# Performance work log

Hardware: AMD Instinct MI355X
Metric: run time of the kernel (lower is better)

The kernel has to match this reference:

```python
import jax, jax.numpy as jnp
import numpy as np
from jax import lax

OBS, ACT, H, VOX = 2264, 32, 4096, 216  # voxel tail is 6*6*6


def _conv3d(v, w, b):
    # v: [1,1,6,6,6], w: [1,1,3,3,3] (OIDHW), SAME padding, stride 1
    y = lax.conv_general_dilated(v, w, window_strides=(1, 1, 1), padding='SAME',
                                 dimension_numbers=('NCDHW', 'OIDHW', 'NCDHW'))
    return jax.nn.relu(y + b.reshape(1, -1, 1, 1, 1))


def setup_inputs() -> dict:
    key = jax.random.key(0)
    ks = jax.random.split(key, 24)
    s = 0.05
    inp = {'x': jax.random.normal(ks[0], (1, OBS), dtype=jnp.float32)}
    # six Conv3d(1,1,3) kernels + biases
    for i in range(6):
        inp[f'cw{i}'] = jax.random.normal(ks[1 + i], (1, 1, 3, 3, 3), dtype=jnp.float32) * s
        inp[f'cb{i}'] = jax.random.normal(ks[7 + i], (1,), dtype=jnp.float32) * s
    # MLP: Linear(OBS->H), Linear(H->H), Linear(H->ACT); torch layout W:[out,in]
    inp['W0'] = jax.random.normal(ks[13], (H, OBS), dtype=jnp.float32) * 0.02
    inp['b0'] = jnp.zeros((H,), jnp.float32)
    inp['W1'] = jax.random.normal(ks[14], (H, H), dtype=jnp.float32) * 0.02
    inp['b1'] = jnp.zeros((H,), jnp.float32)
    inp['W2'] = jax.random.normal(ks[15], (ACT, H), dtype=jnp.float32) * 0.02
    inp['b2'] = jnp.zeros((ACT,), jnp.float32)
    # default transformations (in_shift=0, in_scale=1, out_shift=0, out_scale=1)
    inp['in_shift'] = jnp.zeros((OBS,), jnp.float32)
    inp['in_scale'] = jnp.ones((OBS,), jnp.float32)
    inp['out_shift'] = jnp.zeros((ACT,), jnp.float32)
    inp['out_scale'] = jnp.ones((ACT,), jnp.float32)
    return inp


def reference(x, cw0, cw1, cw2, cw3, cw4, cw5, cb0, cb1, cb2, cb3, cb4, cb5,
              W0, b0, W1, b1, W2, b2, in_shift, in_scale, out_shift, out_scale):
    v = x[:, -VOX:].reshape(1, 1, 6, 6, 6)
    for w, b in ((cw0, cb0), (cw1, cb1), (cw2, cb2), (cw3, cb3), (cw4, cb4), (cw5, cb5)):
        v = _conv3d(v, w, b)
    out = jnp.concatenate([x[:, :-VOX], v.reshape(1, VOX)], axis=1)
    out = (out - in_shift) / (in_scale + 1e-8)
    out = jnp.tanh(out @ W0.T + b0)
    out = jnp.tanh(out @ W1.T + b1)
    out = out @ W2.T + b2
    return out * out_scale + out_shift
```

## Files before the change

### kernel.cpp

```cpp
#include <hip/hip_runtime.h>
#include <math.h>

#define OBS 2264
#define ACT 32
#define HID 4096
#define VOX 216
#define PRE (OBS - VOX)

__global__ __launch_bounds__(256) void conv_norm_kernel(
    const float* __restrict__ x,
    const float* __restrict__ cw0, const float* __restrict__ cb0,
    const float* __restrict__ cw1, const float* __restrict__ cb1,
    const float* __restrict__ cw2, const float* __restrict__ cb2,
    const float* __restrict__ cw3, const float* __restrict__ cb3,
    const float* __restrict__ cw4, const float* __restrict__ cb4,
    const float* __restrict__ cw5, const float* __restrict__ cb5,
    const float* __restrict__ in_shift, const float* __restrict__ in_scale,
    float* __restrict__ u)
{
    __shared__ float vb[2][VOX];
    const int tid = threadIdx.x;

    if (tid < VOX) vb[0][tid] = x[PRE + tid];
    __syncthreads();

    const float* ws[6] = {cw0, cw1, cw2, cw3, cw4, cw5};
    const float* bs[6] = {cb0, cb1, cb2, cb3, cb4, cb5};

    int cur = 0;
    for (int l = 0; l < 6; ++l) {
        float acc = 0.f;
        if (tid < VOX) {
            const int d = tid / 36;
            const int h = (tid / 6) % 6;
            const int w = tid % 6;
            const float* k = ws[l];
            acc = bs[l][0];
            #pragma unroll
            for (int kd = 0; kd < 3; ++kd) {
                const int dd = d + kd - 1;
                if (dd < 0 || dd > 5) continue;
                #pragma unroll
                for (int kh = 0; kh < 3; ++kh) {
                    const int hh = h + kh - 1;
                    if (hh < 0 || hh > 5) continue;
                    #pragma unroll
                    for (int kw = 0; kw < 3; ++kw) {
                        const int ww = w + kw - 1;
                        if (ww < 0 || ww > 5) continue;
                        acc += k[kd * 9 + kh * 3 + kw] * vb[cur][dd * 36 + hh * 6 + ww];
                    }
                }
            }
            acc = fmaxf(acc, 0.f);
            vb[cur ^ 1][tid] = acc;
        }
        cur ^= 1;
        __syncthreads();
    }

    for (int i = tid; i < OBS; i += 256) {
        const float val = (i < PRE) ? x[i] : vb[cur][i - PRE];
        u[i] = (val - in_shift[i]) / (in_scale[i] + 1e-8f);
    }
}

template<int NIN, bool DO_TANH>
__global__ __launch_bounds__(256) void gemv_kernel(
    const float* __restrict__ W, const float* __restrict__ b,
    const float* __restrict__ u, float* __restrict__ out)
{
    constexpr int N4 = NIN / 4;
    const int row = blockIdx.x;
    const int tid = threadIdx.x;
    const float4* __restrict__ Wr = reinterpret_cast<const float4*>(W + (size_t)row * NIN);
    const float4* __restrict__ u4 = reinterpret_cast<const float4*>(u);

    float acc = 0.f;
    for (int j = tid; j < N4; j += 256) {
        const float4 wv = Wr[j];
        const float4 uv = u4[j];
        acc += wv.x * uv.x + wv.y * uv.y + wv.z * uv.z + wv.w * uv.w;
    }
    #pragma unroll
    for (int off = 32; off > 0; off >>= 1) acc += __shfl_down(acc, off, 64);

    __shared__ float part[4];
    if ((tid & 63) == 0) part[tid >> 6] = acc;
    __syncthreads();
    if (tid == 0) {
        float s = part[0] + part[1] + part[2] + part[3] + b[row];
        out[row] = DO_TANH ? tanhf(s) : s;
    }
}

__global__ __launch_bounds__(256) void gemv_out_kernel(
    const float* __restrict__ W, const float* __restrict__ b,
    const float* __restrict__ u,
    const float* __restrict__ oscale, const float* __restrict__ oshift,
    float* __restrict__ out)
{
    constexpr int N4 = HID / 4;
    const int row = blockIdx.x;
    const int tid = threadIdx.x;
    const float4* __restrict__ Wr = reinterpret_cast<const float4*>(W + (size_t)row * HID);
    const float4* __restrict__ u4 = reinterpret_cast<const float4*>(u);

    float acc = 0.f;
    for (int j = tid; j < N4; j += 256) {
        const float4 wv = Wr[j];
        const float4 uv = u4[j];
        acc += wv.x * uv.x + wv.y * uv.y + wv.z * uv.z + wv.w * uv.w;
    }
    #pragma unroll
    for (int off = 32; off > 0; off >>= 1) acc += __shfl_down(acc, off, 64);

    __shared__ float part[4];
    if ((tid & 63) == 0) part[tid >> 6] = acc;
    __syncthreads();
    if (tid == 0) {
        float s = part[0] + part[1] + part[2] + part[3] + b[row];
        out[row] = s * oscale[row] + oshift[row];
    }
}

extern "C" void kernel_launch(void* const* d_in, const int* in_sizes, int n_in,
                              void* d_out, int out_size, void* d_ws, size_t ws_size,
                              hipStream_t stream) {
    const float* x = (const float*)d_in[0];

    const float* cw[6];
    const float* cb[6];
    if (in_sizes[2] == 1) {
        for (int i = 0; i < 6; ++i) {
            cw[i] = (const float*)d_in[1 + 2 * i];
            cb[i] = (const float*)d_in[2 + 2 * i];
        }
    } else {
        for (int i = 0; i < 6; ++i) {
            cw[i] = (const float*)d_in[1 + i];
            cb[i] = (const float*)d_in[7 + i];
        }
    }
    const float* W0       = (const float*)d_in[13];
    const float* b0       = (const float*)d_in[14];
    const float* W1       = (const float*)d_in[15];
    const float* b1       = (const float*)d_in[16];
    const float* W2       = (const float*)d_in[17];
    const float* b2       = (const float*)d_in[18];
    const float* in_shift = (const float*)d_in[19];
    const float* in_scale = (const float*)d_in[20];
    const float* oshift   = (const float*)d_in[21];
    const float* oscale   = (const float*)d_in[22];

    float* ws = (float*)d_ws;
    float* u  = ws;
    float* h0 = ws + 2304;
    float* h1 = ws + 6400;
    float* y  = (float*)d_out;

    conv_norm_kernel<<<1, 256, 0, stream>>>(
        x, cw[0], cb[0], cw[1], cb[1], cw[2], cb[2],
        cw[3], cb[3], cw[4], cb[4], cw[5], cb[5],
        in_shift, in_scale, u);

    gemv_kernel<OBS, true><<<HID, 256, 0, stream>>>(W0, b0, u, h0);
    gemv_kernel<HID, true><<<HID, 256, 0, stream>>>(W1, b1, h0, h1);
    gemv_out_kernel<<<ACT, 256, 0, stream>>>(W2, b2, h1, oscale, oshift, y);
}
```

Measured before the change: 42.32 us.

## Fuse conv/normalization prologue into first GEMV with per-block recompute

The conv3d stack and input normalization are folded into the first GEMV kernel: each of the 4096 blocks recomputes the conv layers and normalized input into shared memory, then does its row dot product. This removes one kernel launch and the global round trip for the normalized vector. The cost is redundant conv and normalization work plus several barriers in every block. The remaining HID-length GEMV loops also get an unroll hint.

```diff
diff --git a/kernel.cpp b/kernel.cpp
--- a/kernel.cpp
+++ b/kernel.cpp
@@ -6,8 +6,10 @@
 #define HID 4096
 #define VOX 216
 #define PRE (OBS - VOX)
+#define N4_OBS (OBS / 4)
+#define N4_HID (HID / 4)
 
-__global__ __launch_bounds__(256) void conv_norm_kernel(
+__global__ __launch_bounds__(256) void fused0_kernel(
     const float* __restrict__ x,
     const float* __restrict__ cw0, const float* __restrict__ cb0,
     const float* __restrict__ cw1, const float* __restrict__ cb1,
@@ -16,9 +18,13 @@
     const float* __restrict__ cw4, const float* __restrict__ cb4,
     const float* __restrict__ cw5, const float* __restrict__ cb5,
     const float* __restrict__ in_shift, const float* __restrict__ in_scale,
-    float* __restrict__ u)
+    const float* __restrict__ W0, const float* __restrict__ b0,
+    float* __restrict__ h0)
 {
     __shared__ float vb[2][VOX];
+    __shared__ __align__(16) float su[OBS];
+    __shared__ float part[4];
+
     const int tid = threadIdx.x;
 
     if (tid < VOX) vb[0][tid] = x[PRE + tid];
@@ -28,14 +34,14 @@
     const float* bs[6] = {cb0, cb1, cb2, cb3, cb4, cb5};
 
     int cur = 0;
+    #pragma unroll 1
     for (int l = 0; l < 6; ++l) {
-        float acc = 0.f;
         if (tid < VOX) {
             const int d = tid / 36;
             const int h = (tid / 6) % 6;
             const int w = tid % 6;
             const float* k = ws[l];
-            acc = bs[l][0];
+            float acc = bs[l][0];
             #pragma unroll
             for (int kd = 0; kd < 3; ++kd) {
                 const int dd = d + kd - 1;
@@ -52,8 +58,7 @@
                     }
                 }
             }
-            acc = fmaxf(acc, 0.f);
-            vb[cur ^ 1][tid] = acc;
+            vb[cur ^ 1][tid] = fmaxf(acc, 0.f);
         }
         cur ^= 1;
         __syncthreads();
@@ -61,23 +66,43 @@
 
     for (int i = tid; i < OBS; i += 256) {
         const float val = (i < PRE) ? x[i] : vb[cur][i - PRE];
-        u[i] = (val - in_shift[i]) / (in_scale[i] + 1e-8f);
+        su[i] = (val - in_shift[i]) / (in_scale[i] + 1e-8f);
+    }
+    __syncthreads();
+
+    const int row = blockIdx.x;
+    const float4* __restrict__ Wr = reinterpret_cast<const float4*>(W0 + (size_t)row * OBS);
+    const float4* __restrict__ u4 = reinterpret_cast<const float4*>(su);
+
+    float acc = 0.f;
+    for (int j = tid; j < N4_OBS; j += 256) {
+        const float4 wv = Wr[j];
+        const float4 uv = u4[j];
+        acc += wv.x * uv.x + wv.y * uv.y + wv.z * uv.z + wv.w * uv.w;
+    }
+    #pragma unroll
+    for (int off = 32; off > 0; off >>= 1) acc += __shfl_down(acc, off, 64);
+
+    if ((tid & 63) == 0) part[tid >> 6] = acc;
+    __syncthreads();
+    if (tid == 0) {
+        const float s = part[0] + part[1] + part[2] + part[3] + b0[row];
+        h0[row] = tanhf(s);
     }
 }
 
-template<int NIN, bool DO_TANH>
-__global__ __launch_bounds__(256) void gemv_kernel(
+__global__ __launch_bounds__(256) void gemv1_kernel(
     const float* __restrict__ W, const float* __restrict__ b,
     const float* __restrict__ u, float* __restrict__ out)
 {
-    constexpr int N4 = NIN / 4;
     const int row = blockIdx.x;
     const int tid = threadIdx.x;
-    const float4* __restrict__ Wr = reinterpret_cast<const float4*>(W + (size_t)row * NIN);
+    const float4* __restrict__ Wr = reinterpret_cast<const float4*>(W + (size_t)row * HID);
     const float4* __restrict__ u4 = reinterpret_cast<const float4*>(u);
 
     float acc = 0.f;
-    for (int j = tid; j < N4; j += 256) {
+    #pragma unroll 4
+    for (int j = tid; j < N4_HID; j += 256) {
         const float4 wv = Wr[j];
         const float4 uv = u4[j];
         acc += wv.x * uv.x + wv.y * uv.y + wv.z * uv.z + wv.w * uv.w;
@@ -89,8 +114,8 @@
     if ((tid & 63) == 0) part[tid >> 6] = acc;
     __syncthreads();
     if (tid == 0) {
-        float s = part[0] + part[1] + part[2] + part[3] + b[row];
-        out[row] = DO_TANH ? tanhf(s) : s;
+        const float s = part[0] + part[1] + part[2] + part[3] + b[row];
+        out[row] = tanhf(s);
     }
 }
 
@@ -100,14 +125,14 @@
     const float* __restrict__ oscale, const float* __restrict__ oshift,
     float* __restrict__ out)
 {
-    constexpr int N4 = HID / 4;
     const int row = blockIdx.x;
     const int tid = threadIdx.x;
     const float4* __restrict__ Wr = reinterpret_cast<const float4*>(W + (size_t)row * HID);
     const float4* __restrict__ u4 = reinterpret_cast<const float4*>(u);
 
     float acc = 0.f;
-    for (int j = tid; j < N4; j += 256) {
+    #pragma unroll 4
+    for (int j = tid; j < N4_HID; j += 256) {
         const float4 wv = Wr[j];
         const float4 uv = u4[j];
         acc += wv.x * uv.x + wv.y * uv.y + wv.z * uv.z + wv.w * uv.w;
@@ -119,7 +144,7 @@
     if ((tid & 63) == 0) part[tid >> 6] = acc;
     __syncthreads();
     if (tid == 0) {
-        float s = part[0] + part[1] + part[2] + part[3] + b[row];
+        const float s = part[0] + part[1] + part[2] + part[3] + b[row];
         out[row] = s * oscale[row] + oshift[row];
     }
 }
@@ -154,17 +179,15 @@
     const float* oscale   = (const float*)d_in[22];
 
     float* ws = (float*)d_ws;
-    float* u  = ws;
-    float* h0 = ws + 2304;
-    float* h1 = ws + 6400;
+    float* h0 = ws;
+    float* h1 = ws + 4096;
     float* y  = (float*)d_out;
 
-    conv_norm_kernel<<<1, 256, 0, stream>>>(
+    fused0_kernel<<<HID, 256, 0, stream>>>(
         x, cw[0], cb[0], cw[1], cb[1], cw[2], cb[2],
         cw[3], cb[3], cw[4], cb[4], cw[5], cb[5],
-        in_shift, in_scale, u);
+        in_shift, in_scale, W0, b0, h0);
 
-    gemv_kernel<OBS, true><<<HID, 256, 0, stream>>>(W0, b0, u, h0);
-    gemv_kernel<HID, true><<<HID, 256, 0, stream>>>(W1, b1, h0, h1);
+    gemv1_kernel<<<HID, 256, 0, stream>>>(W1, b1, h0, h1);
     gemv_out_kernel<<<ACT, 256, 0, stream>>>(W2, b2, h1, oscale, oshift, y);
 }
```

Result: slower. 66.58 us (+57.3%).
